# Kernel tuning notes

Hardware: AMD Instinct MI355X
Metric: run time of the kernel (lower is better)

The kernel has to match this reference:

```python
import jax, jax.numpy as jnp
import numpy as np

B, S, D = 4, 2048, 1024
E = 8            # num_experts
F = 4096         # expert hidden dim (4*D)
T = B * S        # tokens
CAP = 1280       # capacity = ceil(1.25 * T / E)


def setup_inputs() -> dict:
    key = jax.random.key(0)
    k1, k2, k3, k4 = jax.random.split(key, 4)
    inputs = jax.random.normal(k1, (B, S, D), dtype=jnp.float32)
    gate_w = jax.random.normal(k2, (D, E), dtype=jnp.float32) / np.sqrt(D)
    w1 = jax.random.normal(k3, (E, D, F), dtype=jnp.float32) / np.sqrt(D)
    w2 = jax.random.normal(k4, (E, F, D), dtype=jnp.float32) / np.sqrt(F)
    return {"inputs": inputs, "gate_w": gate_w, "w1": w1, "w2": w2}


def reference(inputs, gate_w, w1, w2):
    tokens = inputs.reshape(-1, D)                       # [T, D]
    logits = tokens @ gate_w                             # [T, E] (gate, no bias)
    probs = jax.nn.softmax(logits, axis=-1)
    expert_idx = jnp.argmax(probs, axis=-1)              # top-1 routing
    mask1 = jax.nn.one_hot(expert_idx, E, dtype=tokens.dtype)        # [T, E]
    # position of each token within its chosen expert's queue
    pos = (jnp.cumsum(mask1, axis=0) - 1.0).astype(jnp.int32)        # [T, E]
    # one_hot of out-of-range (>= CAP) positions is all-zero -> capacity drop
    sec_mask = mask1[:, :, None] * jax.nn.one_hot(pos, CAP, dtype=tokens.dtype)  # [T, E, C]
    combine_weights = probs[:, :, None] * sec_mask       # [T, E, C]
    # dispatch: matmul(sec_mask.permute(1,2,0), tokens) -> [E, C, D]
    expert_input = jnp.einsum('tec,td->ecd', sec_mask, tokens)
    # grouped per-expert FFN
    h = jax.nn.relu(jnp.einsum('ecd,edf->ecf', expert_input, w1))    # [E, C, F]
    expert_output = jnp.einsum('ecf,efd->ecd', h, w2)                # [E, C, D]
    # combine: [T, E*C] @ [E*C, D]
    out = jnp.einsum('tec,ecd->td', combine_weights, expert_output)  # [T, D]
    return out.reshape(inputs.shape)
```

## Files before the change

### kernel.cpp

```cpp
#include <hip/hip_runtime.h>
#include <hip/hip_bf16.h>

#define TOKENS   8192
#define DDIM     1024
#define NEXP     8
#define FDIM     4096
#define CAPACITY 1280
#define NYT      10

typedef __attribute__((ext_vector_type(8))) __bf16 bf16x8;
typedef __attribute__((ext_vector_type(4))) __bf16 bf16x4;
typedef __attribute__((ext_vector_type(4))) float  f32x4;

typedef __attribute__((address_space(1))) const void gvoid_t;
typedef __attribute__((address_space(3))) void       lvoid_t;

__device__ __forceinline__ void async16(const void* g, void* l) {
  __builtin_amdgcn_global_load_lds((gvoid_t*)g, (lvoid_t*)l, 16, 0, 0);
}

__global__ void gate_kernel(const float* __restrict__ x, const float* __restrict__ gw,
                            int* __restrict__ eidx, float* __restrict__ prob) {
  const int t = blockIdx.x;
  const int lane = threadIdx.x;
  const float* xp = x + (size_t)t * DDIM;
  float acc[NEXP];
#pragma unroll
  for (int e = 0; e < NEXP; ++e) acc[e] = 0.f;
#pragma unroll 4
  for (int i = 0; i < DDIM / 64; ++i) {
    const int d = i * 64 + lane;
    const float xv = xp[d];
    const f32x4 g0 = *(const f32x4*)(gw + d * NEXP);
    const f32x4 g1 = *(const f32x4*)(gw + d * NEXP + 4);
    acc[0] += xv * g0[0]; acc[1] += xv * g0[1];
    acc[2] += xv * g0[2]; acc[3] += xv * g0[3];
    acc[4] += xv * g1[0]; acc[5] += xv * g1[1];
    acc[6] += xv * g1[2]; acc[7] += xv * g1[3];
  }
#pragma unroll
  for (int e = 0; e < NEXP; ++e) {
    float v = acc[e];
#pragma unroll
    for (int off = 32; off; off >>= 1) v += __shfl_xor(v, off);
    acc[e] = v;
  }
  if (lane == 0) {
    float m = acc[0]; int mi = 0;
#pragma unroll
    for (int e = 1; e < NEXP; ++e) if (acc[e] > m) { m = acc[e]; mi = e; }
    float s = 0.f;
#pragma unroll
    for (int e = 0; e < NEXP; ++e) s += __expf(acc[e] - m);
    eidx[t] = mi;
    prob[t] = 1.f / s;
  }
}

__global__ void scan_kernel(const int* __restrict__ eidx, int* __restrict__ src,
                            int* __restrict__ counts) {
  __shared__ int buf[2][NEXP][256];
  const int tid = threadIdx.x;
  for (int i = tid; i < NEXP * CAPACITY; i += 256) src[i] = -1;
  const int t0 = tid * (TOKENS / 256);
#pragma unroll
  for (int e = 0; e < NEXP; ++e) buf[0][e][tid] = 0;
  for (int k = 0; k < TOKENS / 256; ++k) {
    const int e = eidx[t0 + k];
    buf[0][e][tid]++;
  }
  __syncthreads();
  int cur = 0;
  for (int off = 1; off < 256; off <<= 1) {
#pragma unroll
    for (int e = 0; e < NEXP; ++e) {
      int v = buf[cur][e][tid];
      if (tid >= off) v += buf[cur][e][tid - off];
      buf[cur ^ 1][e][tid] = v;
    }
    __syncthreads();
    cur ^= 1;
  }
  if (tid < NEXP) counts[tid] = buf[cur][tid][255];
#pragma unroll
  for (int e = 0; e < NEXP; ++e)
    buf[cur ^ 1][e][tid] = (tid > 0) ? buf[cur][e][tid - 1] : 0;
  for (int k = 0; k < TOKENS / 256; ++k) {
    const int t = t0 + k;
    const int e = eidx[t];
    const int p = buf[cur ^ 1][e][tid]++;
    if (p < CAPACITY) src[e * CAPACITY + p] = t;
  }
}

__global__ void dispatch_kernel(const float* __restrict__ tokens, const int* __restrict__ src,
                                __bf16* __restrict__ Xb) {
  const int slot = blockIdx.x;
  const int tid  = threadIdx.x;
  const int t = src[slot];
  bf16x4* dst = (bf16x4*)(Xb + (size_t)slot * DDIM);
  bf16x4 o;
  if (t >= 0) {
    const f32x4 v = ((const f32x4*)(tokens + (size_t)t * DDIM))[tid];
    o[0] = (__bf16)v[0]; o[1] = (__bf16)v[1]; o[2] = (__bf16)v[2]; o[3] = (__bf16)v[3];
  } else {
    o[0] = (__bf16)0.f; o[1] = (__bf16)0.f; o[2] = (__bf16)0.f; o[3] = (__bf16)0.f;
  }
  dst[tid] = o;
}

__global__ void transpose_convert_kernel(const float* __restrict__ w, __bf16* __restrict__ wt,
                                         int R, int C) {
  __shared__ __bf16 tile[64][66];
  const int e = blockIdx.z;
  const float* wp = w + (size_t)e * R * C;
  __bf16* op = wt + (size_t)e * R * C;
  const int c0 = blockIdx.x * 64, r0 = blockIdx.y * 64;
  const int tid = threadIdx.x;
#pragma unroll
  for (int p = 0; p < 4; ++p) {
    const int r = p * 16 + (tid >> 4);
    const int c = (tid & 15) * 4;
    const f32x4 v = *(const f32x4*)(wp + (size_t)(r0 + r) * C + c0 + c);
    tile[r][c]     = (__bf16)v[0]; tile[r][c + 1] = (__bf16)v[1];
    tile[r][c + 2] = (__bf16)v[2]; tile[r][c + 3] = (__bf16)v[3];
  }
  __syncthreads();
#pragma unroll
  for (int p = 0; p < 2; ++p) {
    const int c  = p * 32 + (tid >> 3);
    const int rg = (tid & 7) * 8;
    bf16x8 o;
#pragma unroll
    for (int i = 0; i < 8; ++i) o[i] = tile[rg + i][c];
    *(bf16x8*)(op + (size_t)(c0 + c) * R + r0 + rg) = o;
  }
}

__global__ __launch_bounds__(256, 2)
void gemm1_kernel(const __bf16* __restrict__ A, const __bf16* __restrict__ B,
                  __bf16* __restrict__ Cbf, const int* __restrict__ counts,
                  int K, size_t sA, size_t sB, size_t sC) {
  constexpr int N  = FDIM;
  constexpr int NX = N / 128;
  __shared__ __bf16 lds[2][128 * 64];

  const int nwg = NX * NYT * NEXP;
  int wg = blockIdx.x;
  wg = (wg & 7) * (nwg >> 3) + (wg >> 3);
  const int e   = wg / (NX * NYT);
  const int rem = wg - e * (NX * NYT);
  const int ty  = rem % NYT;
  const int tx  = rem / NYT;
  const int m0  = ty * 128, n0 = tx * 128;

  const int cnt   = counts[e];
  const int tiles = (cnt + 127) >> 7;
  if (ty >= ((tiles < NYT) ? tiles : NYT)) return;

  const __bf16* Ae = A + (size_t)e * sA;
  const __bf16* Be = B + (size_t)e * sB;
  const int tid = threadIdx.x;
  const int wid = tid >> 6, lane = tid & 63;
  const int wm = wid >> 1, wn = wid & 1;
  const int rl = lane & 15, gl = lane >> 4;

  f32x4 acc[4][4];
#pragma unroll
  for (int m = 0; m < 4; ++m)
#pragma unroll
    for (int n = 0; n < 4; ++n) acc[m][n] = (f32x4){0.f, 0.f, 0.f, 0.f};

  for (int kt = 0; kt < K; kt += 64) {
#pragma unroll
    for (int i = 0; i < 4; ++i) {
      const int s   = (wid * 4 + i) * 64 + lane;
      const int row = s >> 3;
      const int cg  = (s & 7) ^ (row & 7);
      async16(Ae + (size_t)(m0 + row) * K + kt + cg * 8, &lds[0][(wid * 4 + i) * 512]);
      async16(Be + (size_t)(n0 + row) * K + kt + cg * 8, &lds[1][(wid * 4 + i) * 512]);
    }
    __syncthreads();
    const char* la = (const char*)&lds[0][0];
    const char* lb = (const char*)&lds[1][0];
#pragma unroll
    for (int kk = 0; kk < 2; ++kk) {
      bf16x8 af[4], bv[4];
#pragma unroll
      for (int m = 0; m < 4; ++m) {
        const int rowin = wm * 64 + m * 16 + rl;
        af[m] = *(const bf16x8*)(la + rowin * 128 + (((kk * 4 + gl) ^ (rowin & 7)) * 16));
      }
#pragma unroll
      for (int n = 0; n < 4; ++n) {
        const int rowin = wn * 64 + n * 16 + rl;
        bv[n] = *(const bf16x8*)(lb + rowin * 128 + (((kk * 4 + gl) ^ (rowin & 7)) * 16));
      }
#pragma unroll
      for (int m = 0; m < 4; ++m)
#pragma unroll
        for (int n = 0; n < 4; ++n)
          acc[m][n] = __builtin_amdgcn_mfma_f32_16x16x32_bf16(af[m], bv[n], acc[m][n], 0, 0, 0);
    }
    __syncthreads();
  }

  __bf16* Ce = Cbf + (size_t)e * sC;
#pragma unroll
  for (int m = 0; m < 4; ++m)
#pragma unroll
    for (int j = 0; j < 4; ++j) {
      const int row = m0 + wm * 64 + m * 16 + gl * 4 + j;
#pragma unroll
      for (int n = 0; n < 4; ++n) {
        const int col = n0 + wn * 64 + n * 16 + rl;
        float v = acc[m][n][j];
        v = v > 0.f ? v : 0.f;
        Ce[(size_t)row * N + col] = (__bf16)v;
      }
    }
}

__global__ __launch_bounds__(256, 2)
void gemm2_kernel(const __bf16* __restrict__ A, const float* __restrict__ Bw,
                  float* __restrict__ out, const int* __restrict__ src,
                  const float* __restrict__ prob, const int* __restrict__ counts,
                  int K, size_t sA, size_t sBw) {
  constexpr int N  = DDIM;
  constexpr int NX = N / 128;
  __shared__ __bf16 lds[2][128 * 64];

  const int nwg = NX * NYT * NEXP;
  int wg = blockIdx.x;
  wg = (wg & 7) * (nwg >> 3) + (wg >> 3);
  const int e   = wg / (NX * NYT);
  const int rem = wg - e * (NX * NYT);
  const int ty  = rem % NYT;
  const int tx  = rem / NYT;
  const int m0  = ty * 128, n0 = tx * 128;

  const int cnt   = counts[e];
  const int tiles = (cnt + 127) >> 7;
  if (ty >= ((tiles < NYT) ? tiles : NYT)) return;

  const __bf16* Ae = A + (size_t)e * sA;
  const float*  Be = Bw + (size_t)e * sBw;
  const int tid = threadIdx.x;
  const int wid = tid >> 6, lane = tid & 63;
  const int wm = wid >> 1, wn = wid & 1;
  const int rl = lane & 15, gl = lane >> 4;
  const int nq = tid & 31;
  const int kb = tid >> 5;

  f32x4 acc[4][4];
#pragma unroll
  for (int m = 0; m < 4; ++m)
#pragma unroll
    for (int n = 0; n < 4; ++n) acc[m][n] = (f32x4){0.f, 0.f, 0.f, 0.f};

  for (int kt = 0; kt < K; kt += 64) {
    f32x4 r[8];
#pragma unroll
    for (int i = 0; i < 8; ++i)
      r[i] = *(const f32x4*)(Be + (size_t)(kt + kb * 8 + i) * N + n0 + nq * 4);
#pragma unroll
    for (int i = 0; i < 4; ++i) {
      const int s   = (wid * 4 + i) * 64 + lane;
      const int row = s >> 3;
      const int cg  = (s & 7) ^ (row & 7);
      async16(Ae + (size_t)(m0 + row) * K + kt + cg * 8, &lds[0][(wid * 4 + i) * 512]);
    }
#pragma unroll
    for (int i2 = 0; i2 < 4; ++i2) {
      const int n  = nq * 4 + i2;
      const int sl = kb ^ (n & 7) ^ ((n >> 3) & 7);
      bf16x8 o;
#pragma unroll
      for (int i = 0; i < 8; ++i) o[i] = (__bf16)r[i][i2];
      *(bf16x8*)((char*)&lds[1][0] + n * 128 + sl * 16) = o;
    }
    __syncthreads();
    const char* la = (const char*)&lds[0][0];
    const char* lb = (const char*)&lds[1][0];
#pragma unroll
    for (int kk = 0; kk < 2; ++kk) {
      bf16x8 af[4], bv[4];
#pragma unroll
      for (int m = 0; m < 4; ++m) {
        const int rowin = wm * 64 + m * 16 + rl;
        af[m] = *(const bf16x8*)(la + rowin * 128 + (((kk * 4 + gl) ^ (rowin & 7)) * 16));
      }
#pragma unroll
      for (int n = 0; n < 4; ++n) {
        const int rowin = wn * 64 + n * 16 + rl;
        const int sl = (kk * 4 + gl) ^ (rowin & 7) ^ ((rowin >> 3) & 7);
        bv[n] = *(const bf16x8*)(lb + rowin * 128 + sl * 16);
      }
#pragma unroll
      for (int m = 0; m < 4; ++m)
#pragma unroll
        for (int n = 0; n < 4; ++n)
          acc[m][n] = __builtin_amdgcn_mfma_f32_16x16x32_bf16(af[m], bv[n], acc[m][n], 0, 0, 0);
    }
    __syncthreads();
  }

#pragma unroll
  for (int m = 0; m < 4; ++m)
#pragma unroll
    for (int j = 0; j < 4; ++j) {
      const int slot = m0 + wm * 64 + m * 16 + gl * 4 + j;
      const int t = src[e * CAPACITY + slot];
      if (t >= 0) {
        const float p = prob[t];
        float* op = out + (size_t)t * N;
#pragma unroll
        for (int n = 0; n < 4; ++n) {
          const int col = n0 + wn * 64 + n * 16 + rl;
          op[col] = p * acc[m][n][j];
        }
      }
    }
}

extern "C" void kernel_launch(void* const* d_in, const int* in_sizes, int n_in,
                              void* d_out, int out_size, void* d_ws, size_t ws_size,
                              hipStream_t stream) {
  const float* x  = (const float*)d_in[0];
  const float* gw = (const float*)d_in[1];
  const float* w1 = (const float*)d_in[2];
  const float* w2 = (const float*)d_in[3];
  float* out = (float*)d_out;

  char* ws = (char*)d_ws;
  size_t off = 0;
  auto alloc = [&](size_t bytes) {
    void* p = ws + off;
    off += (bytes + 255) & ~(size_t)255;
    return p;
  };
  __bf16* W1bT = (__bf16*)alloc((size_t)NEXP * FDIM * DDIM * 2);
  __bf16* Xb   = (__bf16*)alloc((size_t)NEXP * CAPACITY * DDIM * 2);
  __bf16* Hb   = (__bf16*)alloc((size_t)NEXP * CAPACITY * FDIM * 2);
  int*   eidx  = (int*)alloc(TOKENS * sizeof(int));
  float* prob  = (float*)alloc(TOKENS * sizeof(float));
  int*   srcm  = (int*)alloc(NEXP * CAPACITY * sizeof(int));
  int*   cnts  = (int*)alloc(NEXP * sizeof(int));
  (void)ws_size; (void)in_sizes; (void)n_in;

  hipMemsetAsync(d_out, 0, (size_t)out_size * sizeof(float), stream);

  gate_kernel<<<TOKENS, 64, 0, stream>>>(x, gw, eidx, prob);
  scan_kernel<<<1, 256, 0, stream>>>(eidx, srcm, cnts);
  dispatch_kernel<<<NEXP * CAPACITY, 256, 0, stream>>>(x, srcm, Xb);
  transpose_convert_kernel<<<dim3(FDIM / 64, DDIM / 64, NEXP), 256, 0, stream>>>(
      w1, W1bT, DDIM, FDIM);
  gemm1_kernel<<<(FDIM / 128) * NYT * NEXP, 256, 0, stream>>>(
      Xb, W1bT, Hb, cnts,
      DDIM, (size_t)CAPACITY * DDIM, (size_t)FDIM * DDIM, (size_t)CAPACITY * FDIM);
  gemm2_kernel<<<(DDIM / 128) * NYT * NEXP, 256, 0, stream>>>(
      Hb, w2, out, srcm, prob, cnts,
      FDIM, (size_t)CAPACITY * FDIM, (size_t)FDIM * DDIM);
}
```

Measured before the change: 305.0 us.

## Pretranspose w2 to bf16 inside gemm1 launch; gemm2 uses async bf16 B loads

Adds a w2 fp32-to-bf16 transpose that shares a launch with the first grouped GEMM. Extra blocks appended after the GEMM tiles do the transpose, so it can fill CUs left idle by early-exiting tiles. The second GEMM now reads pre-transposed bf16 weights with async global-to-LDS loads, instead of converting fp32 w2 in registers on every K step. This removes repeated fp32 weight traffic and conversion work in gemm2, at the cost of an extra bf16 weight buffer and one more full pass over w2.

```diff
diff --git a/kernel.cpp b/kernel.cpp
--- a/kernel.cpp
+++ b/kernel.cpp
@@ -7,6 +7,8 @@
 #define FDIM     4096
 #define CAPACITY 1280
 #define NYT      10
+#define NWG1     ((FDIM / 128) * NYT * NEXP)
+#define NWGT2    ((DDIM / 64) * (FDIM / 64) * NEXP)
 
 typedef __attribute__((ext_vector_type(8))) __bf16 bf16x8;
 typedef __attribute__((ext_vector_type(4))) __bf16 bf16x4;
@@ -138,10 +140,133 @@
 }
 
 __global__ __launch_bounds__(256, 2)
-void gemm1_kernel(const __bf16* __restrict__ A, const __bf16* __restrict__ B,
-                  __bf16* __restrict__ Cbf, const int* __restrict__ counts,
-                  int K, size_t sA, size_t sB, size_t sC) {
-  constexpr int N  = FDIM;
+void fused_g1w2t_kernel(const __bf16* __restrict__ A, const __bf16* __restrict__ B,
+                        __bf16* __restrict__ Cbf, const int* __restrict__ counts,
+                        const float* __restrict__ w2, __bf16* __restrict__ w2t) {
+  __shared__ char smem[32768];
+
+  if (blockIdx.x < NWG1) {
+    constexpr int N  = FDIM;
+    constexpr int NX = N / 128;
+    constexpr int K  = DDIM;
+    __bf16* lds0 = (__bf16*)smem;
+    __bf16* lds1 = (__bf16*)(smem + 16384);
+
+    const int nwg = NX * NYT * NEXP;
+    int wg = blockIdx.x;
+    wg = (wg & 7) * (nwg >> 3) + (wg >> 3);
+    const int e   = wg / (NX * NYT);
+    const int rem = wg - e * (NX * NYT);
+    const int ty  = rem % NYT;
+    const int tx  = rem / NYT;
+    const int m0  = ty * 128, n0 = tx * 128;
+
+    const int cnt   = counts[e];
+    const int tiles = (cnt + 127) >> 7;
+    if (ty >= ((tiles < NYT) ? tiles : NYT)) return;
+
+    const __bf16* Ae = A + (size_t)e * ((size_t)CAPACITY * DDIM);
+    const __bf16* Be = B + (size_t)e * ((size_t)FDIM * DDIM);
+    const int tid = threadIdx.x;
+    const int wid = tid >> 6, lane = tid & 63;
+    const int wm = wid >> 1, wn = wid & 1;
+    const int rl = lane & 15, gl = lane >> 4;
+
+    f32x4 acc[4][4];
+#pragma unroll
+    for (int m = 0; m < 4; ++m)
+#pragma unroll
+      for (int n = 0; n < 4; ++n) acc[m][n] = (f32x4){0.f, 0.f, 0.f, 0.f};
+
+    for (int kt = 0; kt < K; kt += 64) {
+#pragma unroll
+      for (int i = 0; i < 4; ++i) {
+        const int s   = (wid * 4 + i) * 64 + lane;
+        const int row = s >> 3;
+        const int cg  = (s & 7) ^ (row & 7);
+        async16(Ae + (size_t)(m0 + row) * K + kt + cg * 8, &lds0[(wid * 4 + i) * 512]);
+        async16(Be + (size_t)(n0 + row) * K + kt + cg * 8, &lds1[(wid * 4 + i) * 512]);
+      }
+      __syncthreads();
+      const char* la = (const char*)lds0;
+      const char* lb = (const char*)lds1;
+#pragma unroll
+      for (int kk = 0; kk < 2; ++kk) {
+        bf16x8 af[4], bv[4];
+#pragma unroll
+        for (int m = 0; m < 4; ++m) {
+          const int rowin = wm * 64 + m * 16 + rl;
+          af[m] = *(const bf16x8*)(la + rowin * 128 + (((kk * 4 + gl) ^ (rowin & 7)) * 16));
+        }
+#pragma unroll
+        for (int n = 0; n < 4; ++n) {
+          const int rowin = wn * 64 + n * 16 + rl;
+          bv[n] = *(const bf16x8*)(lb + rowin * 128 + (((kk * 4 + gl) ^ (rowin & 7)) * 16));
+        }
+#pragma unroll
+        for (int m = 0; m < 4; ++m)
+#pragma unroll
+          for (int n = 0; n < 4; ++n)
+            acc[m][n] = __builtin_amdgcn_mfma_f32_16x16x32_bf16(af[m], bv[n], acc[m][n], 0, 0, 0);
+      }
+      __syncthreads();
+    }
+
+    __bf16* Ce = Cbf + (size_t)e * ((size_t)CAPACITY * FDIM);
+#pragma unroll
+    for (int m = 0; m < 4; ++m)
+#pragma unroll
+      for (int j = 0; j < 4; ++j) {
+        const int row = m0 + wm * 64 + m * 16 + gl * 4 + j;
+#pragma unroll
+        for (int n = 0; n < 4; ++n) {
+          const int col = n0 + wn * 64 + n * 16 + rl;
+          float v = acc[m][n][j];
+          v = v > 0.f ? v : 0.f;
+          Ce[(size_t)row * N + col] = (__bf16)v;
+        }
+      }
+  } else {
+    constexpr int R = FDIM, C = DDIM;
+    const int idx = blockIdx.x - NWG1;
+    const int e   = idx >> 10;
+    const int rem = idx & 1023;
+    const int by  = rem >> 4;
+    const int bx  = rem & 15;
+    auto tile = [&](int r, int c) -> __bf16& {
+      return *(__bf16*)(smem + ((r * 66 + c) << 1));
+    };
+    const float* wp = w2 + (size_t)e * R * C;
+    __bf16* op = w2t + (size_t)e * R * C;
+    const int c0 = bx * 64, r0 = by * 64;
+    const int tid = threadIdx.x;
+#pragma unroll
+    for (int p = 0; p < 4; ++p) {
+      const int r = p * 16 + (tid >> 4);
+      const int c = (tid & 15) * 4;
+      const f32x4 v = *(const f32x4*)(wp + (size_t)(r0 + r) * C + c0 + c);
+      tile(r, c)     = (__bf16)v[0]; tile(r, c + 1) = (__bf16)v[1];
+      tile(r, c + 2) = (__bf16)v[2]; tile(r, c + 3) = (__bf16)v[3];
+    }
+    __syncthreads();
+#pragma unroll
+    for (int p = 0; p < 2; ++p) {
+      const int c  = p * 32 + (tid >> 3);
+      const int rg = (tid & 7) * 8;
+      bf16x8 o;
+#pragma unroll
+      for (int i = 0; i < 8; ++i) o[i] = tile(rg + i, c);
+      *(bf16x8*)(op + (size_t)(c0 + c) * R + r0 + rg) = o;
+    }
+  }
+}
+
+__global__ __launch_bounds__(256, 2)
+void gemm2_kernel(const __bf16* __restrict__ A, const __bf16* __restrict__ B,
+                  float* __restrict__ out, const int* __restrict__ src,
+                  const float* __restrict__ prob, const int* __restrict__ counts,
+                  int K, size_t sA, size_t sB) {
+  constexpr int N  = DDIM;
   constexpr int NX = N / 128;
   __shared__ __bf16 lds[2][128 * 64];
 
@@ -205,106 +330,6 @@
     __syncthreads();
   }
 
-  __bf16* Ce = Cbf + (size_t)e * sC;
-#pragma unroll
-  for (int m = 0; m < 4; ++m)
-#pragma unroll
-    for (int j = 0; j < 4; ++j) {
-      const int row = m0 + wm * 64 + m * 16 + gl * 4 + j;
-#pragma unroll
-      for (int n = 0; n < 4; ++n) {
-        const int col = n0 + wn * 64 + n * 16 + rl;
-        float v = acc[m][n][j];
-        v = v > 0.f ? v : 0.f;
-        Ce[(size_t)row * N + col] = (__bf16)v;
-      }
-    }
-}
-
-__global__ __launch_bounds__(256, 2)
-void gemm2_kernel(const __bf16* __restrict__ A, const float* __restrict__ Bw,
-                  float* __restrict__ out, const int* __restrict__ src,
-                  const float* __restrict__ prob, const int* __restrict__ counts,
-                  int K, size_t sA, size_t sBw) {
-  constexpr int N  = DDIM;
-  constexpr int NX = N / 128;
-  __shared__ __bf16 lds[2][128 * 64];
-
-  const int nwg = NX * NYT * NEXP;
-  int wg = blockIdx.x;
-  wg = (wg & 7) * (nwg >> 3) + (wg >> 3);
-  const int e   = wg / (NX * NYT);
-  const int rem = wg - e * (NX * NYT);
-  const int ty  = rem % NYT;
-  const int tx  = rem / NYT;
-  const int m0  = ty * 128, n0 = tx * 128;
-
-  const int cnt   = counts[e];
-  const int tiles = (cnt + 127) >> 7;
-  if (ty >= ((tiles < NYT) ? tiles : NYT)) return;
-
-  const __bf16* Ae = A + (size_t)e * sA;
-  const float*  Be = Bw + (size_t)e * sBw;
-  const int tid = threadIdx.x;
-  const int wid = tid >> 6, lane = tid & 63;
-  const int wm = wid >> 1, wn = wid & 1;
-  const int rl = lane & 15, gl = lane >> 4;
-  const int nq = tid & 31;
-  const int kb = tid >> 5;
-
-  f32x4 acc[4][4];
-#pragma unroll
-  for (int m = 0; m < 4; ++m)
-#pragma unroll
-    for (int n = 0; n < 4; ++n) acc[m][n] = (f32x4){0.f, 0.f, 0.f, 0.f};
-
-  for (int kt = 0; kt < K; kt += 64) {
-    f32x4 r[8];
-#pragma unroll
-    for (int i = 0; i < 8; ++i)
-      r[i] = *(const f32x4*)(Be + (size_t)(kt + kb * 8 + i) * N + n0 + nq * 4);
-#pragma unroll
-    for (int i = 0; i < 4; ++i) {
-      const int s   = (wid * 4 + i) * 64 + lane;
-      const int row = s >> 3;
-      const int cg  = (s & 7) ^ (row & 7);
-      async16(Ae + (size_t)(m0 + row) * K + kt + cg * 8, &lds[0][(wid * 4 + i) * 512]);
-    }
-#pragma unroll
-    for (int i2 = 0; i2 < 4; ++i2) {
-      const int n  = nq * 4 + i2;
-      const int sl = kb ^ (n & 7) ^ ((n >> 3) & 7);
-      bf16x8 o;
-#pragma unroll
-      for (int i = 0; i < 8; ++i) o[i] = (__bf16)r[i][i2];
-      *(bf16x8*)((char*)&lds[1][0] + n * 128 + sl * 16) = o;
-    }
-    __syncthreads();
-    const char* la = (const char*)&lds[0][0];
-    const char* lb = (const char*)&lds[1][0];
-#pragma unroll
-    for (int kk = 0; kk < 2; ++kk) {
-      bf16x8 af[4], bv[4];
-#pragma unroll
-      for (int m = 0; m < 4; ++m) {
-        const int rowin = wm * 64 + m * 16 + rl;
-        af[m] = *(const bf16x8*)(la + rowin * 128 + (((kk * 4 + gl) ^ (rowin & 7)) * 16));
-      }
-#pragma unroll
-      for (int n = 0; n < 4; ++n) {
-        const int rowin = wn * 64 + n * 16 + rl;
-        const int sl = (kk * 4 + gl) ^ (rowin & 7) ^ ((rowin >> 3) & 7);
-        bv[n] = *(const bf16x8*)(lb + rowin * 128 + sl * 16);
-      }
-#pragma unroll
-      for (int m = 0; m < 4; ++m)
-#pragma unroll
-        for (int n = 0; n < 4; ++n)
-          acc[m][n] = __builtin_amdgcn_mfma_f32_16x16x32_bf16(af[m], bv[n], acc[m][n], 0, 0, 0);
-    }
-    __syncthreads();
-  }
-
 #pragma unroll
   for (int m = 0; m < 4; ++m)
 #pragma unroll
@@ -340,6 +365,7 @@
     return p;
   };
   __bf16* W1bT = (__bf16*)alloc((size_t)NEXP * FDIM * DDIM * 2);
+  __bf16* W2bT = (__bf16*)alloc((size_t)NEXP * DDIM * FDIM * 2);
   __bf16* Xb   = (__bf16*)alloc((size_t)NEXP * CAPACITY * DDIM * 2);
   __bf16* Hb   = (__bf16*)alloc((size_t)NEXP * CAPACITY * FDIM * 2);
   int*   eidx  = (int*)alloc(TOKENS * sizeof(int));
@@ -355,10 +381,9 @@
   dispatch_kernel<<<NEXP * CAPACITY, 256, 0, stream>>>(x, srcm, Xb);
   transpose_convert_kernel<<<dim3(FDIM / 64, DDIM / 64, NEXP), 256, 0, stream>>>(
       w1, W1bT, DDIM, FDIM);
-  gemm1_kernel<<<(FDIM / 128) * NYT * NEXP, 256, 0, stream>>>(
-      Xb, W1bT, Hb, cnts,
-      DDIM, (size_t)CAPACITY * DDIM, (size_t)FDIM * DDIM, (size_t)CAPACITY * FDIM);
+  fused_g1w2t_kernel<<<NWG1 + NWGT2, 256, 0, stream>>>(
+      Xb, W1bT, Hb, cnts, w2, W2bT);
   gemm2_kernel<<<(DDIM / 128) * NYT * NEXP, 256, 0, stream>>>(
-      Hb, w2, out, srcm, prob, cnts,
-      FDIM, (size_t)CAPACITY * FDIM, (size_t)FDIM * DDIM);
-}
+      Hb, W2bT, out, srcm, prob, cnts,
+      FDIM, (size_t)CAPACITY * FDIM, (size_t)DDIM * FDIM);
+}
```

Measured after the change: 296.3 us. -2.9%, faster.
